# Kernel optimization log

Hardware: AMD Instinct MI355X
Metric: run time of the kernel (lower is better)

## Reference

```python
import jax, jax.numpy as jnp
import numpy as np

E = 32  # embedding_dim
B = 1048576

def setup_inputs() -> dict:
    key = jax.random.key(0)
    ks = jax.random.split(key, 16)
    def p(k, shape, scale=0.1):
        return jax.random.normal(k, shape, dtype=jnp.float32) * scale
    return {
        'x': jax.random.normal(ks[0], (B, 2, 5), dtype=jnp.float32),
        'fc_emb_w': p(ks[1], (E, 5)), 'fc_emb_b': p(ks[2], (E,)),
        'in_proj_w': p(ks[3], (3 * E, E)), 'in_proj_b': p(ks[4], (3 * E,)),
        'out_proj_w': p(ks[5], (E, E)), 'out_proj_b': p(ks[6], (E,)),
        'w_ih': p(ks[7], (E, E)), 'b_ih': p(ks[8], (E,)),
        'w_hh': p(ks[9], (E, E)), 'b_hh': p(ks[10], (E,)),
        'fc_dec_w': p(ks[11], (5, E)), 'fc_dec_b': p(ks[12], (5,)),
        'out_w': p(ks[13], (3, 5)), 'out_b': p(ks[14], (3,)),
    }

def gelu(x):
    return jax.nn.gelu(x, approximate=False)  # torch nn.GELU default (erf)

def reference(x, fc_emb_w, fc_emb_b, in_proj_w, in_proj_b,
              out_proj_w, out_proj_b, w_ih, b_ih, w_hh, b_hh,
              fc_dec_w, fc_dec_b, out_w, out_b):
    # per-token embedding: [B,2,5] -> [B,2,E]
    e = gelu(jnp.einsum('bsi,ei->bse', x, fc_emb_w) + fc_emb_b)
    # single-head self-attention (seq_len=2)
    wq, wk, wv = jnp.split(in_proj_w, 3, axis=0)
    bq, bk, bv = jnp.split(in_proj_b, 3, axis=0)
    q = jnp.einsum('bsd,ed->bse', e, wq) + bq
    k = jnp.einsum('bsd,ed->bse', e, wk) + bk
    v = jnp.einsum('bsd,ed->bse', e, wv) + bv
    scores = jnp.einsum('bqd,bkd->bqk', q, k) / jnp.sqrt(jnp.float32(E))
    attn = jax.nn.softmax(scores, axis=-1)
    o = jnp.einsum('bqk,bkd->bqd', attn, v)
    o = jnp.einsum('bsd,ed->bse', o, out_proj_w) + out_proj_b
    # 2-step tanh RNN, h0 = 0; final hidden state only
    h1 = jnp.tanh(o[:, 0] @ w_ih.T + b_ih + b_hh)
    h2 = jnp.tanh(o[:, 1] @ w_ih.T + b_ih + h1 @ w_hh.T + b_hh)
    # decode
    d = gelu(h2 @ fc_dec_w.T + fc_dec_b)
    return d @ out_w.T + out_b  # [B,3]
```

## Files before the change

### kernel.cpp

```cpp
#include <hip/hip_runtime.h>
#include <math.h>

#define BT 256

typedef _Float16 half2v __attribute__((ext_vector_type(2)));
typedef __fp16   fp16x2 __attribute__((ext_vector_type(2)));
typedef _Float16 half8  __attribute__((ext_vector_type(8)));
typedef float    f32x16 __attribute__((ext_vector_type(16)));

union U4H8 { unsigned int u[4]; half8 h; };

__device__ __forceinline__ half2v u2h(unsigned int u){
  union { unsigned int u; half2v h; } c; c.u = u; return c.h;
}
__device__ __forceinline__ unsigned int h2u(half2v h){
  union { unsigned int u; half2v h; } c; c.h = h; return c.u;
}
__device__ __forceinline__ half2v pkrtz(float a, float b){
  union { fp16x2 f; half2v h; } c;
  c.f = __builtin_amdgcn_cvt_pkrtz(a, b);
  return c.h;
}
__device__ __forceinline__ float fdot2(half2v a, half2v b, float c){
  return __builtin_amdgcn_fdot2(a, b, c, false);
}
__device__ __forceinline__ float frcp(float x){ return __builtin_amdgcn_rcpf(x); }

__device__ __forceinline__ unsigned int pk_rne(float a, float b){
  half2v h; h.x = (_Float16)a; h.y = (_Float16)b; return h2u(h);
}

__device__ __forceinline__ float gelu_erf(float v){
  float z  = v * 0.70710678118654752f;
  float az = fabsf(z);
  float t  = frcp(fmaf(0.47047f, az, 1.0f));
  float poly = t*fmaf(t, fmaf(t, 0.7478556f, -0.0958798f), 0.3480242f);
  float ex = __expf(-az*az);
  float erfv = fmaf(-poly, ex, 1.0f);
  erfv = (z < 0.0f) ? -erfv : erfv;
  return 0.5f*v*(1.0f + erfv);
}
__device__ __forceinline__ float tanh_fast(float v){
  float t = __expf(2.0f*v);
  return 1.0f - 2.0f*frcp(t + 1.0f);
}

__global__ void prep_kernel(const float* __restrict__ inw, const float* __restrict__ inb,
                            const float* __restrict__ opw, const float* __restrict__ opb,
                            const float* __restrict__ wih, const float* __restrict__ bih,
                            const float* __restrict__ bhh, const float* __restrict__ whh,
                            const float* __restrict__ decw, const float* __restrict__ embw,
                            const float* __restrict__ decb,
                            unsigned int* __restrict__ wsu){
  __shared__ float sA[1024], sP[1024], sM[1024], sT[32], sWV[32], sBM[32];
  int tx = threadIdx.x & 31;
  int ty = threadIdx.x >> 5;
  float accA = 0.f, accP = 0.f;
  #pragma unroll
  for (int m = 0; m < 32; m++){
    accA += inw[m*32 + ty] * inw[1024 + m*32 + tx];
    accP += opw[ty*32 + m] * inw[2048 + m*32 + tx];
  }
  sA[ty*32 + tx] = accA;
  sP[ty*32 + tx] = accP;
  if (ty == 0){
    float aw = 0.f;
    #pragma unroll
    for (int m = 0; m < 32; m++) aw += inb[m] * inw[1024 + m*32 + tx];
    sWV[tx] = aw;
  }
  if (ty == 1){
    float at = opb[tx];
    #pragma unroll
    for (int m = 0; m < 32; m++) at += opw[tx*32 + m] * inb[64 + m];
    sT[tx] = at;
  }
  __syncthreads();
  float accM = 0.f;
  #pragma unroll
  for (int m = 0; m < 32; m++) accM += wih[ty*32 + m] * sP[m*32 + tx];
  sM[ty*32 + tx] = accM;
  if (ty == 2){
    float ab = bih[tx] + bhh[tx];
    #pragma unroll
    for (int m = 0; m < 32; m++) ab += wih[tx*32 + m] * sT[m];
    sBM[tx] = ab;
  }
  __syncthreads();
  int t = threadIdx.x;
  if (t < 512){
    int r = t >> 4, c2 = (t & 15)*2;
    wsu[t]        = pk_rne(sA[r*32+c2],  sA[r*32+c2+1]);
    wsu[512 + t]  = pk_rne(sM[r*32+c2],  sM[r*32+c2+1]);
    wsu[1024 + t] = pk_rne(whh[r*32+c2], whh[r*32+c2+1]);
    wsu[1536 + t] = (r < 5) ? pk_rne(decw[r*32+c2], decw[r*32+c2+1]) : 0u;
  } else {
    int q = t - 512;
    if (q < 256){
      int j = q >> 3, cc = (q & 7)*2;
      float a = (cc   < 5) ? embw[j*5+cc]   : 0.f;
      float b = (cc+1 < 5) ? embw[j*5+cc+1] : 0.f;
      wsu[2048 + q] = pk_rne(a, b);
    } else if (q < 272){
      int k = (q - 256)*2;
      wsu[2304 + (q-256)] = pk_rne(sWV[k], sWV[k+1]);
    } else if (q < 304){
      ((float*)wsu)[2320 + (q-272)] = sBM[q-272];
    } else if (q < 336){
      int i = q - 304;
      ((float*)wsu)[2352 + i] = (i < 5) ? decb[i] : 0.f;
    }
  }
}

__device__ __forceinline__ half8 ldfrag(const unsigned int* __restrict__ p){
  U4H8 t; t.u[0]=p[0]; t.u[1]=p[1]; t.u[2]=p[2]; t.u[3]=p[3]; return t.h;
}

struct BF { U4H8 b1, b2; };
__device__ __forceinline__ BF toB(const float* v, bool g){
  unsigned int pk0=h2u(pkrtz(v[0], v[1])),  pk1=h2u(pkrtz(v[2], v[3]));
  unsigned int pk2=h2u(pkrtz(v[4], v[5])),  pk3=h2u(pkrtz(v[6], v[7]));
  unsigned int pk4=h2u(pkrtz(v[8], v[9])),  pk5=h2u(pkrtz(v[10],v[11]));
  unsigned int pk6=h2u(pkrtz(v[12],v[13])), pk7=h2u(pkrtz(v[14],v[15]));
  unsigned int s0 = g?pk0:pk2, s1 = g?pk1:pk3, s2 = g?pk4:pk6, s3 = g?pk5:pk7;
  unsigned int r0 = __shfl_xor(s0,32), r1 = __shfl_xor(s1,32);
  unsigned int r2 = __shfl_xor(s2,32), r3 = __shfl_xor(s3,32);
  BF o;
  o.b1.u[0]=g?r0:pk0; o.b1.u[1]=g?r1:pk1; o.b1.u[2]=g?pk2:r0; o.b1.u[3]=g?pk3:r1;
  o.b2.u[0]=g?r2:pk4; o.b2.u[1]=g?r3:pk5; o.b2.u[2]=g?pk6:r2; o.b2.u[3]=g?pk7:r3;
  return o;
}

__global__ __launch_bounds__(BT) void fused_kernel(
    const float* __restrict__ x,
    const unsigned int* __restrict__ wsu,
    const float* __restrict__ embb,
    const float* __restrict__ outw, const float* __restrict__ outb,
    float* __restrict__ y, int B)
{
  int tid  = threadIdx.x;
  int lane = tid & 63;
  int col  = lane & 31;
  bool g   = (lane >> 5) != 0;
  int grp  = g ? 1 : 0;
  long long base = ((long long)blockIdx.x*(BT/64) + (tid>>6)) * 32;
  if (base >= B) return;
  long long elem = base + col;

  const unsigned int* pA = wsu;
  const unsigned int* pM = wsu + 512;
  const unsigned int* pW = wsu + 1024;
  const unsigned int* pD = wsu + 1536;
  const unsigned int* pE = wsu + 2048;
  const unsigned int* pwv = wsu + 2304;
  const float* bMf = (const float*)(wsu + 2320);
  const float* dbf = (const float*)(wsu + 2352);

  half8 embA = ldfrag(pE + col*8  + grp*4);
  half8 A1   = ldfrag(pA + col*16 + grp*4), A2 = ldfrag(pA + col*16 + 8 + grp*4);
  half8 M1   = ldfrag(pM + col*16 + grp*4), M2 = ldfrag(pM + col*16 + 8 + grp*4);
  half8 W1   = ldfrag(pW + col*16 + grp*4), W2 = ldfrag(pW + col*16 + 8 + grp*4);
  half8 D1   = ldfrag(pD + col*16 + grp*4), D2 = ldfrag(pD + col*16 + 8 + grp*4);
  half2v wv1[4], wv2[4];
  #pragma unroll
  for (int j = 0; j < 4; j++){ wv1[j] = u2h(pwv[4*grp+j]); wv2[j] = u2h(pwv[8+4*grp+j]); }

  f32x16 cb_emb, cb_bM, cb_db;
  #pragma unroll
  for (int i = 0; i < 16; i++){
    int r = (i&3) + 8*(i>>2) + 4*grp;
    cb_emb[i] = embb[r]; cb_bM[i] = bMf[r]; cb_db[i] = dbf[r];
  }

  const float2* xp = (const float2*)(x + elem*10ll);
  float2 p0 = xp[0], p1 = xp[1], p2 = xp[2], p3 = xp[3], p4 = xp[4];
  U4H8 xb0, xb1;
  xb0.u[0] = g ? 0u : h2u(pkrtz(p0.x, p0.y));
  xb0.u[1] = g ? 0u : h2u(pkrtz(p1.x, p1.y));
  xb0.u[2] = g ? 0u : h2u(pkrtz(p2.x, 0.f));
  xb0.u[3] = 0u;
  xb1.u[0] = g ? 0u : h2u(pkrtz(p2.y, p3.x));
  xb1.u[1] = g ? 0u : h2u(pkrtz(p3.y, p4.x));
  xb1.u[2] = g ? 0u : h2u(pkrtz(p4.y, 0.f));
  xb1.u[3] = 0u;

  f32x16 e0D = __builtin_amdgcn_mfma_f32_32x32x16_f16(embA, xb0.h, cb_emb, 0,0,0);
  f32x16 e1D = __builtin_amdgcn_mfma_f32_32x32x16_f16(embA, xb1.h, cb_emb, 0,0,0);
  float e0[16], dl[16];
  #pragma unroll
  for (int i = 0; i < 16; i++){
    float a = gelu_erf(e0D[i]);
    float b = gelu_erf(e1D[i]);
    e0[i] = a; dl[i] = b - a;
  }

  BF e0B = toB(e0, g);
  BF dB  = toB(dl, g);
  f32x16 z16;
  #pragma unroll
  for (int i = 0; i < 16; i++) z16[i] = 0.f;
  f32x16 gD = __builtin_amdgcn_mfma_f32_32x32x16_f16(A1, dB.b1.h, z16, 0,0,0);
  gD = __builtin_amdgcn_mfma_f32_32x32x16_f16(A2, dB.b2.h, gD, 0,0,0);

  float t0 = 0.f, t1 = 0.f, dw = 0.f;
  #pragma unroll
  for (int i = 0; i < 16; i++){ t0 = fmaf(e0[i], gD[i], t0); t1 = fmaf(dl[i], gD[i], t1); }
  #pragma unroll
  for (int j = 0; j < 4; j++){
    dw = fdot2(wv1[j], u2h(dB.b1.u[j]), dw);
    dw = fdot2(wv2[j], u2h(dB.b2.u[j]), dw);
  }
  t0 += __shfl_xor(t0, 32);
  t1 += __shfl_xor(t1, 32);
  dw += __shfl_xor(dw, 32);

  const float iss = 0.17677669529663689f;
  float a01 = frcp(1.0f + __expf(-((t0      + dw)*iss)));
  float a11 = frcp(1.0f + __expf(-((t0 + t1 + dw)*iss)));

  _Float16 q01 = (_Float16)a01, q11 = (_Float16)a11;
  half8 v01 = {q01,q01,q01,q01,q01,q01,q01,q01};
  half8 v11 = {q11,q11,q11,q11,q11,q11,q11,q11};
  half8 c0B1 = dB.b1.h*v01 + e0B.b1.h, c0B2 = dB.b2.h*v01 + e0B.b2.h;
  half8 c1B1 = dB.b1.h*v11 + e0B.b1.h, c1B2 = dB.b2.h*v11 + e0B.b2.h;

  f32x16 h1D = __builtin_amdgcn_mfma_f32_32x32x16_f16(M1, c0B1, cb_bM, 0,0,0);
  h1D = __builtin_amdgcn_mfma_f32_32x32x16_f16(M2, c0B2, h1D, 0,0,0);
  float h1f[16];
  #pragma unroll
  for (int i = 0; i < 16; i++) h1f[i] = tanh_fast(h1D[i]);
  BF h1B = toB(h1f, g);

  f32x16 h2D = __builtin_amdgcn_mfma_f32_32x32x16_f16(M1, c1B1, cb_bM, 0,0,0);
  h2D = __builtin_amdgcn_mfma_f32_32x32x16_f16(M2, c1B2, h2D, 0,0,0);
  h2D = __builtin_amdgcn_mfma_f32_32x32x16_f16(W1, h1B.b1.h, h2D, 0,0,0);
  h2D = __builtin_amdgcn_mfma_f32_32x32x16_f16(W2, h1B.b2.h, h2D, 0,0,0);
  float h2f[16];
  #pragma unroll
  for (int i = 0; i < 16; i++) h2f[i] = tanh_fast(h2D[i]);
  BF h2B = toB(h2f, g);

  f32x16 dvD = __builtin_amdgcn_mfma_f32_32x32x16_f16(D1, h2B.b1.h, cb_db, 0,0,0);
  dvD = __builtin_amdgcn_mfma_f32_32x32x16_f16(D2, h2B.b2.h, dvD, 0,0,0);
  float dv4 = __shfl_xor(dvD[0], 32);

  float d0 = gelu_erf(dvD[0]), d1 = gelu_erf(dvD[1]), d2 = gelu_erf(dvD[2]),
        d3 = gelu_erf(dvD[3]), d4 = gelu_erf(dv4);
  float y0 = outb[0] + outw[0]*d0 + outw[1]*d1 + outw[2]*d2 + outw[3]*d3 + outw[4]*d4;
  float y1 = outb[1] + outw[5]*d0 + outw[6]*d1 + outw[7]*d2 + outw[8]*d3 + outw[9]*d4;
  float y2 = outb[2] + outw[10]*d0 + outw[11]*d1 + outw[12]*d2 + outw[13]*d3 + outw[14]*d4;
  if (lane < 32){
    float* yp = y + elem*3ll;
    yp[0] = y0; yp[1] = y1; yp[2] = y2;
  }
}

extern "C" void kernel_launch(void* const* d_in, const int* in_sizes, int n_in,
                              void* d_out, int out_size, void* d_ws, size_t ws_size,
                              hipStream_t stream){
  const float* x    = (const float*)d_in[0];
  const float* embw = (const float*)d_in[1];
  const float* embb = (const float*)d_in[2];
  const float* inw  = (const float*)d_in[3];
  const float* inb  = (const float*)d_in[4];
  const float* opw  = (const float*)d_in[5];
  const float* opb  = (const float*)d_in[6];
  const float* wih  = (const float*)d_in[7];
  const float* bih  = (const float*)d_in[8];
  const float* whh  = (const float*)d_in[9];
  const float* bhh  = (const float*)d_in[10];
  const float* decw = (const float*)d_in[11];
  const float* decb = (const float*)d_in[12];
  const float* outw = (const float*)d_in[13];
  const float* outb = (const float*)d_in[14];
  float* y = (float*)d_out;
  unsigned int* wsu = (unsigned int*)d_ws;

  int B = in_sizes[0] / 10;
  int elems_per_block = (BT/64)*32;

  prep_kernel<<<1, 1024, 0, stream>>>(inw, inb, opw, opb, wih, bih, bhh,
                                      whh, decw, embw, decb, wsu);
  fused_kernel<<<(B + elems_per_block - 1)/elems_per_block, BT, 0, stream>>>(
      x, wsu, embb, outw, outb, y, B);
}
```

Before: 168.0 us.

## Compute embedding GELU in packed fp16 with polynomial erf approximation

Replaces the per-element fp32 erf-based GELU on the embedding outputs with a packed half2 polynomial GELU, cutting the VALU work on the 32 embedding values per lane. The score dot products move to fdot2 on packed halves, bias vectors load as float4, and the second attention mix is derived from the first. This trades accuracy (fp16 polynomial GELU, fp16 score accumulation inputs) for fewer ALU instructions in a compute-bound kernel.

```diff
diff --git a/kernel.cpp b/kernel.cpp
--- a/kernel.cpp
+++ b/kernel.cpp
@@ -43,6 +43,29 @@
 __device__ __forceinline__ float tanh_fast(float v){
   float t = __expf(2.0f*v);
   return 1.0f - 2.0f*frcp(t + 1.0f);
+}
+
+__device__ __forceinline__ half2v gelu_pk(half2v x){
+  const _Float16 a0 = (_Float16)0.3989423f,  a1 = (_Float16)-0.0663157f,
+                 a2 = (_Float16)0.0096298f,  a3 = (_Float16)-0.00095967f,
+                 a4 = (_Float16)0.000048f,   hp = (_Float16)0.5f,
+                 hn = (_Float16)-0.5f;
+  const half2v A0={a0,a0}, A1={a1,a1}, A2={a2,a2}, A3={a3,a3}, A4={a4,a4};
+  const half2v HP={hp,hp}, HN={hn,hn};
+  half2v t = x*x;
+  half2v q = A4*t + A3;
+  q = q*t + A2;
+  q = q*t + A1;
+  q = q*t + A0;
+  half2v u = x*q;
+#if __has_builtin(__builtin_elementwise_min)
+  u = __builtin_elementwise_max(u, HN);
+  u = __builtin_elementwise_min(u, HP);
+#else
+  u.x = u.x > hp ? hp : (u.x < hn ? hn : u.x);
+  u.y = u.y > hp ? hp : (u.y < hn ? hn : u.y);
+#endif
+  return x*(u + HP);
 }
 
 __global__ void prep_kernel(const float* __restrict__ inw, const float* __restrict__ inb,
@@ -118,18 +141,26 @@
 }
 
 struct BF { U4H8 b1, b2; };
-__device__ __forceinline__ BF toB(const float* v, bool g){
-  unsigned int pk0=h2u(pkrtz(v[0], v[1])),  pk1=h2u(pkrtz(v[2], v[3]));
-  unsigned int pk2=h2u(pkrtz(v[4], v[5])),  pk3=h2u(pkrtz(v[6], v[7]));
-  unsigned int pk4=h2u(pkrtz(v[8], v[9])),  pk5=h2u(pkrtz(v[10],v[11]));
-  unsigned int pk6=h2u(pkrtz(v[12],v[13])), pk7=h2u(pkrtz(v[14],v[15]));
-  unsigned int s0 = g?pk0:pk2, s1 = g?pk1:pk3, s2 = g?pk4:pk6, s3 = g?pk5:pk7;
+__device__ __forceinline__ BF toB_pk(const unsigned int* pk, bool g){
+  unsigned int s0 = g?pk[0]:pk[2], s1 = g?pk[1]:pk[3],
+               s2 = g?pk[4]:pk[6], s3 = g?pk[5]:pk[7];
   unsigned int r0 = __shfl_xor(s0,32), r1 = __shfl_xor(s1,32);
   unsigned int r2 = __shfl_xor(s2,32), r3 = __shfl_xor(s3,32);
   BF o;
-  o.b1.u[0]=g?r0:pk0; o.b1.u[1]=g?r1:pk1; o.b1.u[2]=g?pk2:r0; o.b1.u[3]=g?pk3:r1;
-  o.b2.u[0]=g?r2:pk4; o.b2.u[1]=g?r3:pk5; o.b2.u[2]=g?pk6:r2; o.b2.u[3]=g?pk7:r3;
+  o.b1.u[0]=g?r0:pk[0]; o.b1.u[1]=g?r1:pk[1]; o.b1.u[2]=g?pk[2]:r0; o.b1.u[3]=g?pk[3]:r1;
+  o.b2.u[0]=g?r2:pk[4]; o.b2.u[1]=g?r3:pk[5]; o.b2.u[2]=g?pk[6]:r2; o.b2.u[3]=g?pk[7]:r3;
   return o;
+}
+
+__device__ __forceinline__ f32x16 ldbias(const float* __restrict__ p, int grp){
+  const float4* b = (const float4*)(p + 4*grp);
+  float4 q0 = b[0], q1 = b[2], q2 = b[4], q3 = b[6];
+  f32x16 c;
+  c[0]=q0.x; c[1]=q0.y; c[2]=q0.z; c[3]=q0.w;
+  c[4]=q1.x; c[5]=q1.y; c[6]=q1.z; c[7]=q1.w;
+  c[8]=q2.x; c[9]=q2.y; c[10]=q2.z; c[11]=q2.w;
+  c[12]=q3.x; c[13]=q3.y; c[14]=q3.z; c[15]=q3.w;
+  return c;
 }
 
 __global__ __launch_bounds__(BT) void fused_kernel(
@@ -166,12 +197,9 @@
   #pragma unroll
   for (int j = 0; j < 4; j++){ wv1[j] = u2h(pwv[4*grp+j]); wv2[j] = u2h(pwv[8+4*grp+j]); }
 
-  f32x16 cb_emb, cb_bM, cb_db;
-  #pragma unroll
-  for (int i = 0; i < 16; i++){
-    int r = (i&3) + 8*(i>>2) + 4*grp;
-    cb_emb[i] = embb[r]; cb_bM[i] = bMf[r]; cb_db[i] = dbf[r];
-  }
+  f32x16 cb_emb = ldbias(embb, grp);
+  f32x16 cb_bM  = ldbias(bMf,  grp);
+  f32x16 cb_db  = ldbias(dbf,  grp);
 
   const float2* xp = (const float2*)(x + elem*10ll);
   float2 p0 = xp[0], p1 = xp[1], p2 = xp[2], p3 = xp[3], p4 = xp[4];
@@ -187,16 +215,17 @@
 
   f32x16 e0D = __builtin_amdgcn_mfma_f32_32x32x16_f16(embA, xb0.h, cb_emb, 0,0,0);
   f32x16 e1D = __builtin_amdgcn_mfma_f32_32x32x16_f16(embA, xb1.h, cb_emb, 0,0,0);
-  float e0[16], dl[16];
-  #pragma unroll
-  for (int i = 0; i < 16; i++){
-    float a = gelu_erf(e0D[i]);
-    float b = gelu_erf(e1D[i]);
-    e0[i] = a; dl[i] = b - a;
-  }
-
-  BF e0B = toB(e0, g);
-  BF dB  = toB(dl, g);
+  unsigned int epk[8], dlpk[8];
+  #pragma unroll
+  for (int i = 0; i < 8; i++){
+    half2v e0h = gelu_pk(pkrtz(e0D[2*i], e0D[2*i+1]));
+    half2v e1h = gelu_pk(pkrtz(e1D[2*i], e1D[2*i+1]));
+    epk[i]  = h2u(e0h);
+    dlpk[i] = h2u(e1h - e0h);
+  }
+
+  BF e0B = toB_pk(epk, g);
+  BF dB  = toB_pk(dlpk, g);
   f32x16 z16;
   #pragma unroll
   for (int i = 0; i < 16; i++) z16[i] = 0.f;
@@ -205,7 +234,11 @@
 
   float t0 = 0.f, t1 = 0.f, dw = 0.f;
   #pragma unroll
-  for (int i = 0; i < 16; i++){ t0 = fmaf(e0[i], gD[i], t0); t1 = fmaf(dl[i], gD[i], t1); }
+  for (int i = 0; i < 8; i++){
+    half2v gp = pkrtz(gD[2*i], gD[2*i+1]);
+    t0 = fdot2(u2h(epk[i]),  gp, t0);
+    t1 = fdot2(u2h(dlpk[i]), gp, t1);
+  }
   #pragma unroll
   for (int j = 0; j < 4; j++){
     dw = fdot2(wv1[j], u2h(dB.b1.u[j]), dw);
@@ -219,27 +252,29 @@
   float a01 = frcp(1.0f + __expf(-((t0      + dw)*iss)));
   float a11 = frcp(1.0f + __expf(-((t0 + t1 + dw)*iss)));
 
-  _Float16 q01 = (_Float16)a01, q11 = (_Float16)a11;
+  _Float16 q01 = (_Float16)a01, qda = (_Float16)(a11 - a01);
   half8 v01 = {q01,q01,q01,q01,q01,q01,q01,q01};
-  half8 v11 = {q11,q11,q11,q11,q11,q11,q11,q11};
+  half8 vda = {qda,qda,qda,qda,qda,qda,qda,qda};
   half8 c0B1 = dB.b1.h*v01 + e0B.b1.h, c0B2 = dB.b2.h*v01 + e0B.b2.h;
-  half8 c1B1 = dB.b1.h*v11 + e0B.b1.h, c1B2 = dB.b2.h*v11 + e0B.b2.h;
+  half8 c1B1 = dB.b1.h*vda + c0B1,     c1B2 = dB.b2.h*vda + c0B2;
 
   f32x16 h1D = __builtin_amdgcn_mfma_f32_32x32x16_f16(M1, c0B1, cb_bM, 0,0,0);
   h1D = __builtin_amdgcn_mfma_f32_32x32x16_f16(M2, c0B2, h1D, 0,0,0);
-  float h1f[16];
-  #pragma unroll
-  for (int i = 0; i < 16; i++) h1f[i] = tanh_fast(h1D[i]);
-  BF h1B = toB(h1f, g);
+  unsigned int h1pk[8];
+  #pragma unroll
+  for (int i = 0; i < 8; i++)
+    h1pk[i] = h2u(pkrtz(tanh_fast(h1D[2*i]), tanh_fast(h1D[2*i+1])));
+  BF h1B = toB_pk(h1pk, g);
 
   f32x16 h2D = __builtin_amdgcn_mfma_f32_32x32x16_f16(M1, c1B1, cb_bM, 0,0,0);
   h2D = __builtin_amdgcn_mfma_f32_32x32x16_f16(M2, c1B2, h2D, 0,0,0);
   h2D = __builtin_amdgcn_mfma_f32_32x32x16_f16(W1, h1B.b1.h, h2D, 0,0,0);
   h2D = __builtin_amdgcn_mfma_f32_32x32x16_f16(W2, h1B.b2.h, h2D, 0,0,0);
-  float h2f[16];
-  #pragma unroll
-  for (int i = 0; i < 16; i++) h2f[i] = tanh_fast(h2D[i]);
-  BF h2B = toB(h2f, g);
+  unsigned int h2pk[8];
+  #pragma unroll
+  for (int i = 0; i < 8; i++)
+    h2pk[i] = h2u(pkrtz(tanh_fast(h2D[2*i]), tanh_fast(h2D[2*i+1])));
+  BF h2B = toB_pk(h2pk, g);
 
   f32x16 dvD = __builtin_amdgcn_mfma_f32_32x32x16_f16(D1, h2B.b1.h, cb_db, 0,0,0);
   dvD = __builtin_amdgcn_mfma_f32_32x32x16_f16(D2, h2B.b2.h, dvD, 0,0,0);
```

Measured after the change: 155.6 us. -7.4%, faster.
